# Optimization experiments

Measured on AMD Instinct MI355X. Metric: run time of the kernel, lower is better.

Reference implementation:

```python
import jax, jax.numpy as jnp
import numpy as np

N, D, M = 262144, 64, 256
CLAMP = -1e-9  # clamp_max value for the ray denominator


def setup_inputs() -> dict:
    key = jax.random.key(0)
    kz, kp, ka, kb = jax.random.split(key, 4)
    return {
        "z": jax.random.normal(kz, (N, D), dtype=jnp.float32),
        "pivot": jax.random.normal(kp, (D,), dtype=jnp.float32),
        "At": jax.random.normal(ka, (D, M), dtype=jnp.float32),
        "b": jax.random.normal(kb, (M,), dtype=jnp.float32),
    }


def reference(z, pivot, At, b):
    # sign_arg: [N, M] — signed constraint violation A z - b
    sign_arg = z @ At - b[None, :]
    ind = sign_arg >= 0  # violated constraints
    ray = pivot[None, :] - z  # [N, D] direction toward the interior pivot
    # denominator clamped to <= -1e-9 and detached (constant w.r.t. grads)
    denom = jax.lax.stop_gradient(jnp.minimum(ray @ At, CLAMP))  # [N, M]
    alpha = -sign_arg / denom
    # step size = max over violated constraints (alpha*ind zeros out satisfied ones)
    common_alpha = jnp.max(alpha * ind.astype(alpha.dtype), axis=1)  # [N]
    common_ind = jnp.any(ind, axis=1)  # [N] — move only if some constraint violated
    return z + common_ind[:, None].astype(z.dtype) * (common_alpha[:, None] * ray)
```

## Files before the change

### kernel.cpp

```cpp
#include <hip/hip_runtime.h>

#define DIMK 64
#define MC 256
#define RPB 128
#define NROWS 262144
#define NB (NROWS / RPB)

typedef _Float16 half8 __attribute__((ext_vector_type(8)));
typedef _Float16 half4 __attribute__((ext_vector_type(4)));
typedef _Float16 half2v __attribute__((ext_vector_type(2)));
typedef float f32x16 __attribute__((ext_vector_type(16)));

#define ZH_OFF 0
#define ZL_OFF 16384
#define AH_OFF 32768
#define AL_OFF 49152
#define LDS_BYTES 65536

__global__ void precompute_c(const float* __restrict__ pivot,
                             const float* __restrict__ At,
                             float* __restrict__ cvec) {
    const int t = threadIdx.x;
    float acc = 0.f;
#pragma unroll
    for (int k = 0; k < DIMK; ++k) acc = fmaf(pivot[k], At[k * MC + t], acc);
    cvec[t] = acc;
}

__global__ __launch_bounds__(256, 2)
void fused_constrain_mfma(const float* __restrict__ z,
                          const float* __restrict__ pivot,
                          const float* __restrict__ At,
                          const float* __restrict__ b,
                          const float* __restrict__ cvec,
                          float* __restrict__ out) {
    extern __shared__ char lds[];
    const int tid  = threadIdx.x;
    const int lane = tid & 63;
    const int li   = lane & 31;
    const int hi   = lane >> 5;
    const int R0   = (tid >> 6) * 32;
    const int base = blockIdx.x * (RPB * DIMK);

    {
        const float4* __restrict__ src = (const float4*)(z + base);
#pragma unroll
        for (int p = 0; p < 8; ++p) {
            const int f  = p * 256 + tid;
            const int r  = f >> 4;
            const int c4 = f & 15;
            const float4 v = src[f];
            half4 h, l;
            h[0] = (_Float16)v.x; l[0] = (_Float16)(v.x - (float)h[0]);
            h[1] = (_Float16)v.y; l[1] = (_Float16)(v.y - (float)h[1]);
            h[2] = (_Float16)v.z; l[2] = (_Float16)(v.z - (float)h[2]);
            h[3] = (_Float16)v.w; l[3] = (_Float16)(v.w - (float)h[3]);
            const int bo = r * 128 + (((c4 >> 1) ^ (r & 7)) << 4) + ((c4 & 1) << 3);
            *(half4*)(lds + ZH_OFF + bo) = h;
            *(half4*)(lds + ZL_OFF + bo) = l;
        }
    }

    auto stage_at = [&](const int ph) {
        const int n  = tid;
        const int kb = ph * 32;
#pragma unroll
        for (int kc = 0; kc < 4; ++kc) {
            float v[8];
#pragma unroll
            for (int j = 0; j < 8; ++j)
                v[j] = At[(kb + kc * 8 + j) * MC + n];
            half8 h, l;
#pragma unroll
            for (int j = 0; j < 8; ++j) {
                h[j] = (_Float16)v[j];
                l[j] = (_Float16)(v[j] - (float)h[j]);
            }
            const int bo = n * 64 + ((kc ^ (n & 3) ^ ((n >> 2) & 3)) << 4);
            *(half8*)(lds + AH_OFF + bo) = h;
            *(half8*)(lds + AL_OFF + bo) = l;
        }
    };

    f32x16 acc[8];
#pragma unroll
    for (int ct = 0; ct < 8; ++ct)
#pragma unroll
        for (int e = 0; e < 16; ++e) acc[ct][e] = 0.f;

    stage_at(0);
    __syncthreads();

    const int rowA = R0 + li;
    const int zrb  = rowA * 128;
    const int sA   = rowA & 7;
    const int nx   = (li & 3) ^ ((li >> 2) & 3);

    auto compute2 = [&](const int ksBase) {
#pragma unroll
        for (int ksl = 0; ksl < 2; ++ksl) {
            const int ks = ksBase + ksl;
            const int ca = ((ks * 2 + hi) ^ sA) << 4;
            const half8 azh = *(const half8*)(lds + ZH_OFF + zrb + ca);
            const half8 azl = *(const half8*)(lds + ZL_OFF + zrb + ca);
            const int cb = ((ksl * 2 + hi) ^ nx) << 4;
#pragma unroll
            for (int ct = 0; ct < 8; ++ct) {
                const int n = ct * 32 + li;
                const half8 bh = *(const half8*)(lds + AH_OFF + n * 64 + cb);
                const half8 bl = *(const half8*)(lds + AL_OFF + n * 64 + cb);
                acc[ct] = __builtin_amdgcn_mfma_f32_32x32x16_f16(azh, bh, acc[ct], 0, 0, 0);
                acc[ct] = __builtin_amdgcn_mfma_f32_32x32x16_f16(azh, bl, acc[ct], 0, 0, 0);
                acc[ct] = __builtin_amdgcn_mfma_f32_32x32x16_f16(azl, bh, acc[ct], 0, 0, 0);
            }
        }
    };

    compute2(0);
    __syncthreads();
    stage_at(1);
    __syncthreads();
    compute2(2);

    float bv[8], cv[8];
#pragma unroll
    for (int ct = 0; ct < 8; ++ct) {
        bv[ct] = b[ct * 32 + li];
        cv[ct] = cvec[ct * 32 + li];
    }
    float gm[16];
#pragma unroll
    for (int r = 0; r < 16; ++r) gm[r] = 0.f;
#pragma unroll
    for (int ct = 0; ct < 8; ++ct)
#pragma unroll
        for (int r = 0; r < 16; ++r) {
            const float s  = acc[ct][r];
            const float sa = s - bv[ct];
            const float q  = fmaxf(s - cv[ct], 1e-9f);
            gm[r] = fmaxf(gm[r], sa * __builtin_amdgcn_rcpf(q));
        }
#pragma unroll
    for (int r = 0; r < 16; ++r)
#pragma unroll
        for (int off = 1; off < 32; off <<= 1)
            gm[r] = fmaxf(gm[r], __shfl_xor(gm[r], off));

    const float pv0 = pivot[2 * li];
    const float pv1 = pivot[2 * li + 1];
#pragma unroll
    for (int r = 0; r < 16; ++r) {
        const int rl  = (r & 3) + ((r >> 2) << 3) + (hi << 2);
        const int row = R0 + rl;
        const int zb  = row * 128 + (((li >> 2) ^ (row & 7)) << 4) + ((li & 3) << 2);
        const half2v h2 = *(const half2v*)(lds + ZH_OFF + zb);
        const half2v l2 = *(const half2v*)(lds + ZL_OFF + zb);
        const float z0 = (float)h2[0] + (float)l2[0];
        const float z1 = (float)h2[1] + (float)l2[1];
        const float g  = gm[r];
        float2 o;
        o.x = fmaf(g, pv0 - z0, z0);
        o.y = fmaf(g, pv1 - z1, z1);
        *(float2*)(out + base + row * 64 + 2 * li) = o;
    }
}

extern "C" void kernel_launch(void* const* d_in, const int* in_sizes, int n_in,
                              void* d_out, int out_size, void* d_ws, size_t ws_size,
                              hipStream_t stream) {
    const float* z     = (const float*)d_in[0];
    const float* pivot = (const float*)d_in[1];
    const float* At    = (const float*)d_in[2];
    const float* b     = (const float*)d_in[3];
    float* cvec = (float*)d_ws;
    precompute_c<<<dim3(1), dim3(MC), 0, stream>>>(pivot, At, cvec);
    fused_constrain_mfma<<<dim3(NB), dim3(256), LDS_BYTES, stream>>>(
        z, pivot, At, b, cvec, (float*)d_out);
}
```

Measured before the change: 167.3 us.

## Pre-split At once, shrink blocks, keep z in registers, split columns across waves

A one-block pre-kernel converts At into swizzled fp16 hi/lo tiles in workspace, so each block does a plain copy instead of converting At itself. Blocks drop from 128 to 64 rows, and each pair of waves splits the 256 columns, so the per-wave row max is combined through a small LDS buffer. z is loaded straight into registers as MFMA A-fragments instead of being staged in LDS. The epilogue re-reads z from global memory. LDS use falls to about 33 KB and the launch bound allows 4 blocks per CU, which should raise occupancy, at the cost of an extra sync and a second read of z.

```diff
diff --git a/kernel.cpp b/kernel.cpp
--- a/kernel.cpp
+++ b/kernel.cpp
@@ -2,143 +2,197 @@
 
 #define DIMK 64
 #define MC 256
-#define RPB 128
+#define BR 64
 #define NROWS 262144
-#define NB (NROWS / RPB)
+#define NB (NROWS / BR)
+
+#define WS_AT 1024
+#define WS_NEED (1024 + 65536)
+
+#define LDS_AH 0
+#define LDS_AL 16384
+#define LDS_GM 32768
 
 typedef _Float16 half8 __attribute__((ext_vector_type(8)));
-typedef _Float16 half4 __attribute__((ext_vector_type(4)));
-typedef _Float16 half2v __attribute__((ext_vector_type(2)));
 typedef float f32x16 __attribute__((ext_vector_type(16)));
-
-#define ZH_OFF 0
-#define ZL_OFF 16384
-#define AH_OFF 32768
-#define AL_OFF 49152
-#define LDS_BYTES 65536
 
 __global__ void precompute_c(const float* __restrict__ pivot,
                              const float* __restrict__ At,
-                             float* __restrict__ cvec) {
+                             float* __restrict__ ws) {
     const int t = threadIdx.x;
     float acc = 0.f;
 #pragma unroll
     for (int k = 0; k < DIMK; ++k) acc = fmaf(pivot[k], At[k * MC + t], acc);
-    cvec[t] = acc;
-}
-
-__global__ __launch_bounds__(256, 2)
+    ws[t] = acc;
+}
+
+__global__ void precompute_at(const float* __restrict__ pivot,
+                              const float* __restrict__ At,
+                              float* __restrict__ ws) {
+    const int t = threadIdx.x;
+    const int swz = (t & 3) ^ ((t >> 2) & 3);
+    float col[DIMK];
+    float acc = 0.f;
+#pragma unroll
+    for (int k = 0; k < DIMK; ++k) {
+        col[k] = At[k * MC + t];
+        acc = fmaf(pivot[k], col[k], acc);
+    }
+    ws[t] = acc;
+    char* wsb = (char*)ws;
+#pragma unroll
+    for (int s = 0; s < 2; ++s) {
+#pragma unroll
+        for (int kc = 0; kc < 4; ++kc) {
+            half8 h, l;
+#pragma unroll
+            for (int j = 0; j < 8; ++j) {
+                const float v = col[s * 32 + kc * 8 + j];
+                h[j] = (_Float16)v;
+                l[j] = (_Float16)(v - (float)h[j]);
+            }
+            const int off = t * 64 + ((kc ^ swz) << 4);
+            *(half8*)(wsb + WS_AT + s * 32768 + off) = h;
+            *(half8*)(wsb + WS_AT + s * 32768 + 16384 + off) = l;
+        }
+    }
+}
+
+template <bool PREAT>
+__global__ __launch_bounds__(256, 4)
 void fused_constrain_mfma(const float* __restrict__ z,
                           const float* __restrict__ pivot,
                           const float* __restrict__ At,
                           const float* __restrict__ b,
-                          const float* __restrict__ cvec,
+                          const float* __restrict__ ws,
                           float* __restrict__ out) {
-    extern __shared__ char lds[];
+    __shared__ __align__(16) char lds[33280];
+
     const int tid  = threadIdx.x;
     const int lane = tid & 63;
     const int li   = lane & 31;
     const int hi   = lane >> 5;
-    const int R0   = (tid >> 6) * 32;
-    const int base = blockIdx.x * (RPB * DIMK);
-
+    const int wid  = tid >> 6;
+    const int rg   = wid >> 1;
+    const int cg   = wid & 1;
+    const int R0   = rg * 32;
+    const int colbase = cg * 128;
+    const int swz  = (li & 3) ^ ((li >> 2) & 3);
+    const int base = blockIdx.x * (BR * DIMK);
+
+    auto stage_at = [&](const int s) {
+        if constexpr (PREAT) {
+            const char* wsA = (const char*)ws + WS_AT + s * 32768;
+#pragma unroll
+            for (int p = 0; p < 8; ++p) {
+                const int f = p * 256 + tid;
+                *(float4*)(lds + f * 16) = *(const float4*)(wsA + f * 16);
+            }
+        } else {
+            const int swzT = (tid & 3) ^ ((tid >> 2) & 3);
+#pragma unroll
+            for (int kc = 0; kc < 4; ++kc) {
+                float v[8];
+#pragma unroll
+                for (int j = 0; j < 8; ++j)
+                    v[j] = At[(s * 32 + kc * 8 + j) * MC + tid];
+                half8 h, l;
+#pragma unroll
+                for (int j = 0; j < 8; ++j) {
+                    h[j] = (_Float16)v[j];
+                    l[j] = (_Float16)(v[j] - (float)h[j]);
+                }
+                const int off = tid * 64 + ((kc ^ swzT) << 4);
+                *(half8*)(lds + LDS_AH + off) = h;
+                *(half8*)(lds + LDS_AL + off) = l;
+            }
+        }
+    };
+
+    float4 zf[8];
     {
-        const float4* __restrict__ src = (const float4*)(z + base);
-#pragma unroll
-        for (int p = 0; p < 8; ++p) {
-            const int f  = p * 256 + tid;
-            const int r  = f >> 4;
-            const int c4 = f & 15;
-            const float4 v = src[f];
-            half4 h, l;
-            h[0] = (_Float16)v.x; l[0] = (_Float16)(v.x - (float)h[0]);
-            h[1] = (_Float16)v.y; l[1] = (_Float16)(v.y - (float)h[1]);
-            h[2] = (_Float16)v.z; l[2] = (_Float16)(v.z - (float)h[2]);
-            h[3] = (_Float16)v.w; l[3] = (_Float16)(v.w - (float)h[3]);
-            const int bo = r * 128 + (((c4 >> 1) ^ (r & 7)) << 4) + ((c4 & 1) << 3);
-            *(half4*)(lds + ZH_OFF + bo) = h;
-            *(half4*)(lds + ZL_OFF + bo) = l;
-        }
-    }
-
-    auto stage_at = [&](const int ph) {
-        const int n  = tid;
-        const int kb = ph * 32;
-#pragma unroll
-        for (int kc = 0; kc < 4; ++kc) {
-            float v[8];
-#pragma unroll
-            for (int j = 0; j < 8; ++j)
-                v[j] = At[(kb + kc * 8 + j) * MC + n];
-            half8 h, l;
-#pragma unroll
-            for (int j = 0; j < 8; ++j) {
-                h[j] = (_Float16)v[j];
-                l[j] = (_Float16)(v[j] - (float)h[j]);
-            }
-            const int bo = n * 64 + ((kc ^ (n & 3) ^ ((n >> 2) & 3)) << 4);
-            *(half8*)(lds + AH_OFF + bo) = h;
-            *(half8*)(lds + AL_OFF + bo) = l;
-        }
-    };
-
-    f32x16 acc[8];
-#pragma unroll
-    for (int ct = 0; ct < 8; ++ct)
+        const float* zr = z + base + (R0 + li) * DIMK + hi * 8;
+#pragma unroll
+        for (int q = 0; q < 4; ++q) {
+            const float* p = zr + (q >> 1) * 32 + (q & 1) * 16;
+            zf[q * 2 + 0] = *(const float4*)(p);
+            zf[q * 2 + 1] = *(const float4*)(p + 4);
+        }
+    }
+
+    stage_at(0);
+
+    half8 azh[4], azl[4];
+    const float* zv = (const float*)zf;
+#pragma unroll
+    for (int q = 0; q < 4; ++q)
+#pragma unroll
+        for (int j = 0; j < 8; ++j) {
+            const float v = zv[q * 8 + j];
+            azh[q][j] = (_Float16)v;
+            azl[q][j] = (_Float16)(v - (float)azh[q][j]);
+        }
+
+    f32x16 acc[4];
+#pragma unroll
+    for (int ct = 0; ct < 4; ++ct)
 #pragma unroll
         for (int e = 0; e < 16; ++e) acc[ct][e] = 0.f;
 
-    stage_at(0);
-    __syncthreads();
-
-    const int rowA = R0 + li;
-    const int zrb  = rowA * 128;
-    const int sA   = rowA & 7;
-    const int nx   = (li & 3) ^ ((li >> 2) & 3);
-
-    auto compute2 = [&](const int ksBase) {
-#pragma unroll
-        for (int ksl = 0; ksl < 2; ++ksl) {
-            const int ks = ksBase + ksl;
-            const int ca = ((ks * 2 + hi) ^ sA) << 4;
-            const half8 azh = *(const half8*)(lds + ZH_OFF + zrb + ca);
-            const half8 azl = *(const half8*)(lds + ZL_OFF + zrb + ca);
-            const int cb = ((ksl * 2 + hi) ^ nx) << 4;
-#pragma unroll
-            for (int ct = 0; ct < 8; ++ct) {
-                const int n = ct * 32 + li;
-                const half8 bh = *(const half8*)(lds + AH_OFF + n * 64 + cb);
-                const half8 bl = *(const half8*)(lds + AL_OFF + n * 64 + cb);
-                acc[ct] = __builtin_amdgcn_mfma_f32_32x32x16_f16(azh, bh, acc[ct], 0, 0, 0);
-                acc[ct] = __builtin_amdgcn_mfma_f32_32x32x16_f16(azh, bl, acc[ct], 0, 0, 0);
-                acc[ct] = __builtin_amdgcn_mfma_f32_32x32x16_f16(azl, bh, acc[ct], 0, 0, 0);
-            }
-        }
-    };
-
-    compute2(0);
-    __syncthreads();
+    __syncthreads();
+
+#pragma unroll
+    for (int ksl = 0; ksl < 2; ++ksl) {
+        const int cb = ((ksl * 2 + hi) ^ swz) << 4;
+        const half8 ah = azh[ksl], al = azl[ksl];
+#pragma unroll
+        for (int ct = 0; ct < 4; ++ct) {
+            const int off = (colbase + ct * 32 + li) * 64 + cb;
+            const half8 bh = *(const half8*)(lds + LDS_AH + off);
+            const half8 bl = *(const half8*)(lds + LDS_AL + off);
+            acc[ct] = __builtin_amdgcn_mfma_f32_32x32x16_f16(ah, bh, acc[ct], 0, 0, 0);
+            acc[ct] = __builtin_amdgcn_mfma_f32_32x32x16_f16(ah, bl, acc[ct], 0, 0, 0);
+            acc[ct] = __builtin_amdgcn_mfma_f32_32x32x16_f16(al, bh, acc[ct], 0, 0, 0);
+        }
+    }
+    __syncthreads();
+
     stage_at(1);
     __syncthreads();
-    compute2(2);
-
-    float bv[8], cv[8];
-#pragma unroll
-    for (int ct = 0; ct < 8; ++ct) {
-        bv[ct] = b[ct * 32 + li];
-        cv[ct] = cvec[ct * 32 + li];
+
+#pragma unroll
+    for (int ksl = 0; ksl < 2; ++ksl) {
+        const int cb = ((ksl * 2 + hi) ^ swz) << 4;
+        const half8 ah = azh[2 + ksl], al = azl[2 + ksl];
+#pragma unroll
+        for (int ct = 0; ct < 4; ++ct) {
+            const int off = (colbase + ct * 32 + li) * 64 + cb;
+            const half8 bh = *(const half8*)(lds + LDS_AH + off);
+            const half8 bl = *(const half8*)(lds + LDS_AL + off);
+            acc[ct] = __builtin_amdgcn_mfma_f32_32x32x16_f16(ah, bh, acc[ct], 0, 0, 0);
+            acc[ct] = __builtin_amdgcn_mfma_f32_32x32x16_f16(ah, bl, acc[ct], 0, 0, 0);
+            acc[ct] = __builtin_amdgcn_mfma_f32_32x32x16_f16(al, bh, acc[ct], 0, 0, 0);
+        }
+    }
+
+    float bv[4], cv[4];
+#pragma unroll
+    for (int ct = 0; ct < 4; ++ct) {
+        const int c = colbase + ct * 32 + li;
+        bv[ct] = b[c];
+        cv[ct] = ws[c];
     }
     float gm[16];
 #pragma unroll
     for (int r = 0; r < 16; ++r) gm[r] = 0.f;
 #pragma unroll
-    for (int ct = 0; ct < 8; ++ct)
+    for (int ct = 0; ct < 4; ++ct)
 #pragma unroll
         for (int r = 0; r < 16; ++r) {
-            const float s  = acc[ct][r];
-            const float sa = s - bv[ct];
-            const float q  = fmaxf(s - cv[ct], 1e-9f);
-            gm[r] = fmaxf(gm[r], sa * __builtin_amdgcn_rcpf(q));
+            const float sv = acc[ct][r];
+            const float sa = sv - bv[ct];
+            const float qd = fmaxf(sv - cv[ct], 1e-9f);
+            gm[r] = fmaxf(gm[r], sa * __builtin_amdgcn_rcpf(qd));
         }
 #pragma unroll
     for (int r = 0; r < 16; ++r)
@@ -146,22 +200,27 @@
         for (int off = 1; off < 32; off <<= 1)
             gm[r] = fmaxf(gm[r], __shfl_xor(gm[r], off));
 
-    const float pv0 = pivot[2 * li];
-    const float pv1 = pivot[2 * li + 1];
+    float* gmbuf = (float*)(lds + LDS_GM);
 #pragma unroll
     for (int r = 0; r < 16; ++r) {
-        const int rl  = (r & 3) + ((r >> 2) << 3) + (hi << 2);
-        const int row = R0 + rl;
-        const int zb  = row * 128 + (((li >> 2) ^ (row & 7)) << 4) + ((li & 3) << 2);
-        const half2v h2 = *(const half2v*)(lds + ZH_OFF + zb);
-        const half2v l2 = *(const half2v*)(lds + ZL_OFF + zb);
-        const float z0 = (float)h2[0] + (float)l2[0];
-        const float z1 = (float)h2[1] + (float)l2[1];
-        const float g  = gm[r];
+        const int row = (r & 3) + 8 * (r >> 2) + 4 * hi;
+        if (li == 0) gmbuf[rg * 64 + row * 2 + cg] = gm[r];
+    }
+    __syncthreads();
+
+    const float2 p2 = *(const float2*)(pivot + 2 * li);
+    const int r0 = cg * 8;
+#pragma unroll
+    for (int rr = 0; rr < 8; ++rr) {
+        const int r   = r0 + rr;
+        const int row = (r & 3) + 8 * (r >> 2) + 4 * hi;
+        const float g = fmaxf(gm[r], gmbuf[rg * 64 + row * 2 + (cg ^ 1)]);
+        const int idx = base + (R0 + row) * DIMK + 2 * li;
+        const float2 zz = *(const float2*)(z + idx);
         float2 o;
-        o.x = fmaf(g, pv0 - z0, z0);
-        o.y = fmaf(g, pv1 - z1, z1);
-        *(float2*)(out + base + row * 64 + 2 * li) = o;
+        o.x = fmaf(g, p2.x - zz.x, zz.x);
+        o.y = fmaf(g, p2.y - zz.y, zz.y);
+        *(float2*)(out + idx) = o;
     }
 }
 
@@ -172,8 +231,14 @@
     const float* pivot = (const float*)d_in[1];
     const float* At    = (const float*)d_in[2];
     const float* b     = (const float*)d_in[3];
-    float* cvec = (float*)d_ws;
-    precompute_c<<<dim3(1), dim3(MC), 0, stream>>>(pivot, At, cvec);
-    fused_constrain_mfma<<<dim3(NB), dim3(256), LDS_BYTES, stream>>>(
-        z, pivot, At, b, cvec, (float*)d_out);
-}
+    float* ws = (float*)d_ws;
+    if (ws_size >= (size_t)WS_NEED) {
+        precompute_at<<<dim3(1), dim3(MC), 0, stream>>>(pivot, At, ws);
+        fused_constrain_mfma<true><<<dim3(NB), dim3(256), 0, stream>>>(
+            z, pivot, At, b, ws, (float*)d_out);
+    } else {
+        precompute_c<<<dim3(1), dim3(MC), 0, stream>>>(pivot, At, ws);
+        fused_constrain_mfma<false><<<dim3(NB), dim3(256), 0, stream>>>(
+            z, pivot, At, b, ws, (float*)d_out);
+    }
+}
```

After: 152.6 us. 8.8% less time.
